# Performance work log

Hardware: AMD Instinct MI355X
Metric: run time of the kernel (lower is better)

The kernel has to match this reference:

```python
import jax, jax.numpy as jnp
import numpy as np

D_MODEL = 1024
N_HEAD = 16
D_K = D_MODEL // N_HEAD
SEQ_LEN = 2048
BATCH = 2
NEG = -1e8


def setup_inputs() -> dict:
    key = jax.random.key(0)
    ks = jax.random.split(key, 8)
    scale = 1.0 / np.sqrt(D_MODEL)
    inp = {
        "input": jax.random.normal(ks[0], (BATCH, SEQ_LEN, D_MODEL), dtype=jnp.float32),
        "mask": jax.random.randint(ks[1], (BATCH, SEQ_LEN), 0, 2) == 1,  # True = masked
        "Wq": jax.random.uniform(ks[2], (D_MODEL, D_MODEL), jnp.float32, -scale, scale),
        "bq": jax.random.uniform(ks[3], (D_MODEL,), jnp.float32, -scale, scale),
        "Wk": jax.random.uniform(ks[4], (D_MODEL, D_MODEL), jnp.float32, -scale, scale),
        "bk": jax.random.uniform(ks[5], (D_MODEL,), jnp.float32, -scale, scale),
        "Wv": jax.random.uniform(ks[6], (D_MODEL, D_MODEL), jnp.float32, -scale, scale),
        "bv": jax.random.uniform(ks[7], (D_MODEL,), jnp.float32, -scale, scale),
    }
    return inp


def reference(input, mask, Wq, bq, Wk, bk, Wv, bv):
    B, S, D = input.shape
    # nn.Linear: y = x @ W^T + b
    def split_heads(x):
        return x.reshape(B, S, N_HEAD, D_K).transpose(0, 2, 1, 3)  # [B,H,S,d_k]

    Q = split_heads(input @ Wq.T + bq)
    K = split_heads(input @ Wk.T + bk)
    V = split_heads(input @ Wv.T + bv)

    scores = jnp.einsum('bhqd,bhkd->bhqk', Q, K) / jnp.sqrt(jnp.float32(D_K))
    # mask [B,S] broadcast over heads and query positions (key mask)
    scores = jnp.where(mask[:, None, None, :], NEG, scores)
    attn = jax.nn.softmax(scores, axis=-1)
    out = jnp.einsum('bhqk,bhkd->bhqd', attn, V)  # [B,H,S,d_k]
    return out.transpose(0, 2, 1, 3).reshape(B, S, D)
```

## Files before the change

### kernel.cpp

```cpp
#include <hip/hip_runtime.h>
#include <hip/hip_bf16.h>
#include <math.h>

#define D_MODEL 1024
#define NH 16
#define DK 64
#define SEQ 2048
#define BATCH 2
#define MTOT (BATCH * SEQ)

typedef unsigned short u16;
typedef unsigned int u32;
typedef short bf16x8 __attribute__((ext_vector_type(8)));
typedef short bf16x4 __attribute__((ext_vector_type(4)));
typedef float f32x4 __attribute__((ext_vector_type(4)));

static constexpr float NEGV2 = -1e8f * 1.44269504089f;
static constexpr float SCL2  = 0.125f * 1.44269504089f;

__device__ __forceinline__ u16 f2bf(float f) {
    union { float f; u32 u; } v; v.f = f;
    u32 r = v.u + 0x7FFFu + ((v.u >> 16) & 1u);
    return (u16)(r >> 16);
}

__device__ __forceinline__ float fexp2(float x) {
#if __has_builtin(__builtin_amdgcn_exp2f)
    return __builtin_amdgcn_exp2f(x);
#else
    return __expf(x * 0.69314718056f);
#endif
}

__device__ __forceinline__ u32 pack2(float lo, float hi) {
    union { __hip_bfloat162 h; u32 u; } cv;
    cv.h = __float22bfloat162_rn(float2{lo, hi});
    return cv.u;
}

__device__ __forceinline__ f32x4 mfma16(bf16x4 a, bf16x4 b, f32x4 c) {
#if __has_builtin(__builtin_amdgcn_mfma_f32_16x16x16_bf16)
    return __builtin_amdgcn_mfma_f32_16x16x16_bf16(a, b, c, 0, 0, 0);
#else
    return __builtin_amdgcn_mfma_f32_16x16x16bf16_1k(a, b, c, 0, 0, 0);
#endif
}

__device__ __forceinline__ void stage16(const u16* g, u16* lds_per_lane) {
#if __has_builtin(__builtin_amdgcn_global_load_lds)
    __builtin_amdgcn_global_load_lds((const __attribute__((address_space(1))) u32*)g,
                                     (__attribute__((address_space(3))) u32*)lds_per_lane,
                                     16, 0, 0);
#else
    *(uint4*)lds_per_lane = *(const uint4*)g;
#endif
}

__global__ __launch_bounds__(256) void convert_bf16(
    const float* __restrict__ X, const float* __restrict__ Wq,
    const float* __restrict__ Wk, const float* __restrict__ Wv,
    u16* __restrict__ Xb, u16* __restrict__ Wb)
{
    const int NX = MTOT * D_MODEL / 4;
    const int NW = D_MODEL * D_MODEL / 4;
    int i = blockIdx.x * 256 + threadIdx.x;
    if (i >= NX + 3 * NW) return;
    float4 v; u16* dst;
    if (i < NX)             { v = ((const float4*)X )[i];            dst = Xb + (size_t)i * 4; }
    else if (i < NX + NW)   { v = ((const float4*)Wq)[i - NX];       dst = Wb + (size_t)(i - NX) * 4; }
    else if (i < NX + 2*NW) { v = ((const float4*)Wk)[i - NX - NW];  dst = Wb + (size_t)NW * 4 + (size_t)(i - NX - NW) * 4; }
    else                    { v = ((const float4*)Wv)[i - NX - 2*NW];dst = Wb + (size_t)NW * 8 + (size_t)(i - NX - 2*NW) * 4; }
    ushort4 o;
    o.x = f2bf(v.x); o.y = f2bf(v.y); o.z = f2bf(v.z); o.w = f2bf(v.w);
    *(ushort4*)dst = o;
}

__global__ __launch_bounds__(256, 2) void proj_mfma(
    const u16* __restrict__ Xb, const u16* __restrict__ Wb,
    const float* __restrict__ bq, const float* __restrict__ bk, const float* __restrict__ bv,
    u16* __restrict__ Qb, u16* __restrict__ Kb, u16* __restrict__ Vb)
{
    __shared__ u16 As[128 * 32];
    __shared__ u16 Bs[128 * 32];

    const int which = blockIdx.z;
    const u16* __restrict__ W = Wb + (size_t)which * D_MODEL * D_MODEL;
    const float* __restrict__ bias = which == 0 ? bq : (which == 1 ? bk : bv);
    u16* __restrict__ Out = which == 0 ? Qb : (which == 1 ? Kb : Vb);

    const int m0 = blockIdx.x * 128, n0 = blockIdx.y * 128;
    const int tid = threadIdx.x, lane = tid & 63, w = tid >> 6;
    const int quad = lane >> 4, l15 = lane & 15;
    const int wr = w >> 1, wc = w & 1;

    f32x4 acc[4][4];
#pragma unroll
    for (int i = 0; i < 4; i++)
#pragma unroll
        for (int j = 0; j < 4; j++) acc[i][j] = (f32x4)0.0f;

    const int srow = 32 * w + (lane >> 2);
    const int scol = (lane & 3) * 8;

    for (int k0 = 0; k0 < D_MODEL; k0 += 32) {
#pragma unroll
        for (int t = 0; t < 2; t++) {
            stage16(Xb + (size_t)(m0 + srow + 16 * t) * D_MODEL + k0 + scol,
                    &As[(32 * w + 16 * t) * 32 + lane * 8]);
            stage16(W + (size_t)(n0 + srow + 16 * t) * D_MODEL + k0 + scol,
                    &Bs[(32 * w + 16 * t) * 32 + lane * 8]);
        }
        __syncthreads();
        bf16x8 af[4], bfr[4];
#pragma unroll
        for (int i = 0; i < 4; i++)
            af[i] = *(const bf16x8*)&As[(wr * 64 + i * 16 + l15) * 32 + quad * 8];
#pragma unroll
        for (int j = 0; j < 4; j++)
            bfr[j] = *(const bf16x8*)&Bs[(wc * 64 + j * 16 + l15) * 32 + quad * 8];
#pragma unroll
        for (int i = 0; i < 4; i++)
#pragma unroll
            for (int j = 0; j < 4; j++)
                acc[i][j] = __builtin_amdgcn_mfma_f32_16x16x32_bf16(af[i], bfr[j], acc[i][j], 0, 0, 0);
        __syncthreads();
    }

    float bj[4];
#pragma unroll
    for (int j = 0; j < 4; j++) bj[j] = bias[n0 + wc * 64 + j * 16 + l15];
#pragma unroll
    for (int i = 0; i < 4; i++) {
#pragma unroll
        for (int j = 0; j < 4; j++) {
#pragma unroll
            for (int r = 0; r < 4; r++) {
                int m = m0 + wr * 64 + i * 16 + quad * 4 + r;
                int n = n0 + wc * 64 + j * 16 + l15;
                int b = m >> 11, s = m & (SEQ - 1);
                int h = n >> 6, d = n & 63;
                Out[(((size_t)b * NH + h) * SEQ + s) * DK + d] = f2bf(acc[i][j][r] + bj[j]);
            }
        }
    }
}

__global__ __launch_bounds__(256, 2) void attn_mfma(
    const u16* __restrict__ Qg, const u16* __restrict__ Kg, const u16* __restrict__ Vg,
    const int* __restrict__ mask, float* __restrict__ out)
{
    constexpr int PADK = 72, PADV = 72;
    __shared__ u16 Ks[2][64 * PADK];
    __shared__ u16 Vt[2][64 * PADV];
    __shared__ float mads[SEQ];

    const int qt0 = blockIdx.x, h = blockIdx.y, b = blockIdx.z;
    const int tid = threadIdx.x, lane = tid & 63, w = tid >> 6;
    const int quad = lane >> 4, l15 = lane & 15;
    const size_t bh = (size_t)b * NH + h;
    const u16* __restrict__ Qp = Qg + (bh * SEQ + qt0 * 128) * DK;
    const u16* __restrict__ Kp = Kg + bh * SEQ * DK;
    const u16* __restrict__ Vp = Vg + bh * SEQ * DK;
    const int* __restrict__ mp = mask + b * SEQ;

    for (int i = tid; i < SEQ; i += 256) mads[i] = mp[i] ? NEGV2 : 0.0f;

    const int q0 = w * 32;
    bf16x8 qf[2][2];
#pragma unroll
    for (int qt = 0; qt < 2; qt++)
#pragma unroll
        for (int half = 0; half < 2; half++)
            qf[qt][half] = *(const bf16x8*)(Qp + (size_t)(q0 + qt * 16 + l15) * DK + half * 32 + quad * 8);

    const int skey = tid & 63, sdk = (tid >> 6) * 16;
    const int vkp2 = (tid & 31) * 2, vd0 = (tid >> 5) * 8;

    {
        const u16* kr = Kp + (size_t)skey * DK + sdk;
        bf16x8 k0 = *(const bf16x8*)kr, k1 = *(const bf16x8*)(kr + 8);
        u16* kd = &Ks[0][skey * PADK + sdk];
        *(bf16x8*)kd = k0; *(bf16x8*)(kd + 8) = k1;
        const u16* vr = Vp + (size_t)vkp2 * DK + vd0;
        bf16x8 v0 = *(const bf16x8*)vr, v1 = *(const bf16x8*)(vr + DK);
#pragma unroll
        for (int i = 0; i < 8; i++)
            *(u32*)&Vt[0][(vd0 + i) * PADV + vkp2] = (u32)(u16)v0[i] | ((u32)(u16)v1[i] << 16);
    }
    __syncthreads();

    f32x4 O[4][2];
    f32x4 sacc[2];
#pragma unroll
    for (int dt = 0; dt < 4; dt++)
#pragma unroll
        for (int qt = 0; qt < 2; qt++) O[dt][qt] = (f32x4)0.0f;
    sacc[0] = (f32x4)0.0f; sacc[1] = (f32x4)0.0f;

    for (int kt = 0; kt < SEQ / 64; kt++) {
        const int bb = kt & 1;
        bf16x8 nk0, nk1, nv0, nv1;
        if (kt < SEQ / 64 - 1) {
            const u16* kr = Kp + (size_t)((kt + 1) * 64 + skey) * DK + sdk;
            nk0 = *(const bf16x8*)kr; nk1 = *(const bf16x8*)(kr + 8);
            const u16* vr = Vp + (size_t)((kt + 1) * 64 + vkp2) * DK + vd0;
            nv0 = *(const bf16x8*)vr; nv1 = *(const bf16x8*)(vr + DK);
        }

        f32x4 St[4][2];
#pragma unroll
        for (int ktl = 0; ktl < 4; ktl++) {
            bf16x8 kf0 = *(const bf16x8*)&Ks[bb][(ktl * 16 + l15) * PADK + quad * 8];
            bf16x8 kf1 = *(const bf16x8*)&Ks[bb][(ktl * 16 + l15) * PADK + 32 + quad * 8];
#pragma unroll
            for (int qt = 0; qt < 2; qt++) {
                f32x4 acc = (f32x4)0.0f;
                acc = __builtin_amdgcn_mfma_f32_16x16x32_bf16(kf0, qf[qt][0], acc, 0, 0, 0);
                acc = __builtin_amdgcn_mfma_f32_16x16x32_bf16(kf1, qf[qt][1], acc, 0, 0, 0);
                St[ktl][qt] = acc;
            }
        }

#pragma unroll
        for (int ktl = 0; ktl < 4; ktl++) {
            f32x4 ma = *(const f32x4*)&mads[kt * 64 + ktl * 16 + quad * 4];
#pragma unroll
            for (int qt = 0; qt < 2; qt++)
#pragma unroll
                for (int r = 0; r < 4; r++) {
                    float p = fexp2(St[ktl][qt][r] * SCL2 + ma[r]);
                    St[ktl][qt][r] = p;
                    sacc[qt][r] += p;
                }
        }

        bf16x4 pf[4][2];
#pragma unroll
        for (int ktl = 0; ktl < 4; ktl++)
#pragma unroll
            for (int qt = 0; qt < 2; qt++) {
                union { u32 u[2]; bf16x4 v; } pu;
                pu.u[0] = pack2(St[ktl][qt][0], St[ktl][qt][1]);
                pu.u[1] = pack2(St[ktl][qt][2], St[ktl][qt][3]);
                pf[ktl][qt] = pu.v;
            }

#pragma unroll
        for (int ktl = 0; ktl < 4; ktl++)
#pragma unroll
            for (int dt = 0; dt < 4; dt++) {
                bf16x4 vf = *(const bf16x4*)&Vt[bb][(dt * 16 + l15) * PADV + ktl * 16 + quad * 4];
#pragma unroll
                for (int qt = 0; qt < 2; qt++)
                    O[dt][qt] = mfma16(vf, pf[ktl][qt], O[dt][qt]);
            }

        if (kt < SEQ / 64 - 1) {
            u16* kd = &Ks[bb ^ 1][skey * PADK + sdk];
            *(bf16x8*)kd = nk0; *(bf16x8*)(kd + 8) = nk1;
#pragma unroll
            for (int i = 0; i < 8; i++)
                *(u32*)&Vt[bb ^ 1][(vd0 + i) * PADV + vkp2] = (u32)(u16)nv0[i] | ((u32)(u16)nv1[i] << 16);
        }
        __syncthreads();
    }

    float inv[2];
#pragma unroll
    for (int qt = 0; qt < 2; qt++) {
        float s = (sacc[qt][0] + sacc[qt][1]) + (sacc[qt][2] + sacc[qt][3]);
        s += __shfl_xor(s, 16);
        s += __shfl_xor(s, 32);
        inv[qt] = 1.0f / s;
    }
#pragma unroll
    for (int qt = 0; qt < 2; qt++) {
        int q = qt0 * 128 + q0 + qt * 16 + l15;
        float* op = out + ((size_t)b * SEQ + q) * D_MODEL + h * DK;
#pragma unroll
        for (int dt = 0; dt < 4; dt++)
#pragma unroll
            for (int r = 0; r < 4; r++)
                op[dt * 16 + quad * 4 + r] = O[dt][qt][r] * inv[qt];
    }
}

extern "C" void kernel_launch(void* const* d_in, const int* in_sizes, int n_in,
                              void* d_out, int out_size, void* d_ws, size_t ws_size,
                              hipStream_t stream)
{
    const float* X  = (const float*)d_in[0];
    const int* mask = (const int*)d_in[1];
    const float* Wq = (const float*)d_in[2];
    const float* bq = (const float*)d_in[3];
    const float* Wk = (const float*)d_in[4];
    const float* bk = (const float*)d_in[5];
    const float* Wv = (const float*)d_in[6];
    const float* bv = (const float*)d_in[7];
    float* out = (float*)d_out;

    u16* Xb = (u16*)d_ws;
    u16* Wb = Xb + (size_t)MTOT * D_MODEL;
    u16* Qb = Wb + (size_t)3 * D_MODEL * D_MODEL;
    u16* Kb = Qb + (size_t)BATCH * NH * SEQ * DK;
    u16* Vb = Kb + (size_t)BATCH * NH * SEQ * DK;

    const int ncvt = (MTOT * D_MODEL + 3 * D_MODEL * D_MODEL) / 4;
    convert_bf16<<<(ncvt + 255) / 256, 256, 0, stream>>>(X, Wq, Wk, Wv, Xb, Wb);
    proj_mfma<<<dim3(MTOT / 128, D_MODEL / 128, 3), 256, 0, stream>>>(Xb, Wb, bq, bk, bv, Qb, Kb, Vb);
    attn_mfma<<<dim3(SEQ / 128, NH, BATCH), 256, 0, stream>>>(Qb, Kb, Vb, mask, out);
}
```

Measured before the change: 174.6 us.

## Shrink attention blocks to 64 queries, precompute mask bias, swizzle projection grid

```diff
diff --git a/kernel.cpp b/kernel.cpp
--- a/kernel.cpp
+++ b/kernel.cpp
@@ -59,12 +59,23 @@
 __global__ __launch_bounds__(256) void convert_bf16(
     const float* __restrict__ X, const float* __restrict__ Wq,
     const float* __restrict__ Wk, const float* __restrict__ Wv,
-    u16* __restrict__ Xb, u16* __restrict__ Wb)
+    const int* __restrict__ mask,
+    u16* __restrict__ Xb, u16* __restrict__ Wb, float* __restrict__ madsg)
 {
     const int NX = MTOT * D_MODEL / 4;
     const int NW = D_MODEL * D_MODEL / 4;
+    const int NM = MTOT / 4;
     int i = blockIdx.x * 256 + threadIdx.x;
-    if (i >= NX + 3 * NW) return;
+    if (i >= NX + 3 * NW + NM) return;
+    if (i >= NX + 3 * NW) {
+        int j = i - NX - 3 * NW;
+        int4 mi = ((const int4*)mask)[j];
+        float4 o;
+        o.x = mi.x ? NEGV2 : 0.0f; o.y = mi.y ? NEGV2 : 0.0f;
+        o.z = mi.z ? NEGV2 : 0.0f; o.w = mi.w ? NEGV2 : 0.0f;
+        ((float4*)madsg)[j] = o;
+        return;
+    }
     float4 v; u16* dst;
     if (i < NX)             { v = ((const float4*)X )[i];            dst = Xb + (size_t)i * 4; }
     else if (i < NX + NW)   { v = ((const float4*)Wq)[i - NX];       dst = Wb + (size_t)(i - NX) * 4; }
@@ -83,12 +94,17 @@
     __shared__ u16 As[128 * 32];
     __shared__ u16 Bs[128 * 32];
 
-    const int which = blockIdx.z;
-    const u16* __restrict__ W = Wb + (size_t)which * D_MODEL * D_MODEL;
-    const float* __restrict__ bias = which == 0 ? bq : (which == 1 ? bk : bv);
-    u16* __restrict__ Out = which == 0 ? Qb : (which == 1 ? Kb : Vb);
-
-    const int m0 = blockIdx.x * 128, n0 = blockIdx.y * 128;
+    const int id = blockIdx.x + 32 * blockIdx.y + 256 * blockIdx.z;
+    const int swz = (id & 7) * 96 + (id >> 3);
+    const int xm = swz & 31;
+    const int yn = (swz >> 5) & 7;
+    const int zi = swz >> 8;
+
+    const u16* __restrict__ W = Wb + (size_t)zi * D_MODEL * D_MODEL;
+    const float* __restrict__ bias = zi == 0 ? bq : (zi == 1 ? bk : bv);
+    u16* __restrict__ Out = zi == 0 ? Qb : (zi == 1 ? Kb : Vb);
+
+    const int m0 = xm * 128, n0 = yn * 128;
     const int tid = threadIdx.x, lane = tid & 63, w = tid >> 6;
     const int quad = lane >> 4, l15 = lane & 15;
     const int wr = w >> 1, wc = w & 1;
@@ -145,25 +161,22 @@
     }
 }
 
-__global__ __launch_bounds__(256, 2) void attn_mfma(
+__global__ __launch_bounds__(128, 2) void attn_mfma(
     const u16* __restrict__ Qg, const u16* __restrict__ Kg, const u16* __restrict__ Vg,
-    const int* __restrict__ mask, float* __restrict__ out)
+    const float* __restrict__ madsg, float* __restrict__ out)
 {
     constexpr int PADK = 72, PADV = 72;
     __shared__ u16 Ks[2][64 * PADK];
     __shared__ u16 Vt[2][64 * PADV];
-    __shared__ float mads[SEQ];
 
     const int qt0 = blockIdx.x, h = blockIdx.y, b = blockIdx.z;
     const int tid = threadIdx.x, lane = tid & 63, w = tid >> 6;
     const int quad = lane >> 4, l15 = lane & 15;
     const size_t bh = (size_t)b * NH + h;
-    const u16* __restrict__ Qp = Qg + (bh * SEQ + qt0 * 128) * DK;
+    const u16* __restrict__ Qp = Qg + (bh * SEQ + qt0 * 64) * DK;
     const u16* __restrict__ Kp = Kg + bh * SEQ * DK;
     const u16* __restrict__ Vp = Vg + bh * SEQ * DK;
-    const int* __restrict__ mp = mask + b * SEQ;
-
-    for (int i = tid; i < SEQ; i += 256) mads[i] = mp[i] ? NEGV2 : 0.0f;
+    const float* __restrict__ mp = madsg + b * SEQ;
 
     const int q0 = w * 32;
     bf16x8 qf[2][2];
@@ -173,19 +186,22 @@
         for (int half = 0; half < 2; half++)
             qf[qt][half] = *(const bf16x8*)(Qp + (size_t)(q0 + qt * 16 + l15) * DK + half * 32 + quad * 8);
 
-    const int skey = tid & 63, sdk = (tid >> 6) * 16;
-    const int vkp2 = (tid & 31) * 2, vd0 = (tid >> 5) * 8;
+    const int skey = tid & 63, sdk = (tid >> 6) * 32;
+    const int vkp2 = (tid & 31) * 2, vd0 = (tid >> 5) * 16;
 
     {
         const u16* kr = Kp + (size_t)skey * DK + sdk;
-        bf16x8 k0 = *(const bf16x8*)kr, k1 = *(const bf16x8*)(kr + 8);
-        u16* kd = &Ks[0][skey * PADK + sdk];
-        *(bf16x8*)kd = k0; *(bf16x8*)(kd + 8) = k1;
+#pragma unroll
+        for (int j = 0; j < 4; j++)
+            *(bf16x8*)&Ks[0][skey * PADK + sdk + 8 * j] = *(const bf16x8*)(kr + 8 * j);
         const u16* vr = Vp + (size_t)vkp2 * DK + vd0;
-        bf16x8 v0 = *(const bf16x8*)vr, v1 = *(const bf16x8*)(vr + DK);
-#pragma unroll
-        for (int i = 0; i < 8; i++)
-            *(u32*)&Vt[0][(vd0 + i) * PADV + vkp2] = (u32)(u16)v0[i] | ((u32)(u16)v1[i] << 16);
+        bf16x8 v0a = *(const bf16x8*)vr,        v0b = *(const bf16x8*)(vr + 8);
+        bf16x8 v1a = *(const bf16x8*)(vr + DK), v1b = *(const bf16x8*)(vr + DK + 8);
+#pragma unroll
+        for (int i = 0; i < 8; i++) {
+            *(u32*)&Vt[0][(vd0 + i) * PADV + vkp2]     = (u32)(u16)v0a[i] | ((u32)(u16)v1a[i] << 16);
+            *(u32*)&Vt[0][(vd0 + 8 + i) * PADV + vkp2] = (u32)(u16)v0b[i] | ((u32)(u16)v1b[i] << 16);
+        }
     }
     __syncthreads();
 
@@ -199,12 +215,14 @@
 
     for (int kt = 0; kt < SEQ / 64; kt++) {
         const int bb = kt & 1;
-        bf16x8 nk0, nk1, nv0, nv1;
+        bf16x8 nk[4], nv0a, nv0b, nv1a, nv1b;
         if (kt < SEQ / 64 - 1) {
             const u16* kr = Kp + (size_t)((kt + 1) * 64 + skey) * DK + sdk;
-            nk0 = *(const bf16x8*)kr; nk1 = *(const bf16x8*)(kr + 8);
+#pragma unroll
+            for (int j = 0; j < 4; j++) nk[j] = *(const bf16x8*)(kr + 8 * j);
             const u16* vr = Vp + (size_t)((kt + 1) * 64 + vkp2) * DK + vd0;
-            nv0 = *(const bf16x8*)vr; nv1 = *(const bf16x8*)(vr + DK);
+            nv0a = *(const bf16x8*)vr;        nv0b = *(const bf16x8*)(vr + 8);
+            nv1a = *(const bf16x8*)(vr + DK); nv1b = *(const bf16x8*)(vr + DK + 8);
         }
 
         f32x4 St[4][2];
@@ -223,7 +241,7 @@
 
 #pragma unroll
         for (int ktl = 0; ktl < 4; ktl++) {
-            f32x4 ma = *(const f32x4*)&mads[kt * 64 + ktl * 16 + quad * 4];
+            f32x4 ma = *(const f32x4*)&mp[kt * 64 + ktl * 16 + quad * 4];
 #pragma unroll
             for (int qt = 0; qt < 2; qt++)
 #pragma unroll
@@ -256,11 +274,14 @@
             }
 
         if (kt < SEQ / 64 - 1) {
-            u16* kd = &Ks[bb ^ 1][skey * PADK + sdk];
-            *(bf16x8*)kd = nk0; *(bf16x8*)(kd + 8) = nk1;
-#pragma unroll
-            for (int i = 0; i < 8; i++)
-                *(u32*)&Vt[bb ^ 1][(vd0 + i) * PADV + vkp2] = (u32)(u16)nv0[i] | ((u32)(u16)nv1[i] << 16);
+#pragma unroll
+            for (int j = 0; j < 4; j++)
+                *(bf16x8*)&Ks[bb ^ 1][skey * PADK + sdk + 8 * j] = nk[j];
+#pragma unroll
+            for (int i = 0; i < 8; i++) {
+                *(u32*)&Vt[bb ^ 1][(vd0 + i) * PADV + vkp2]     = (u32)(u16)nv0a[i] | ((u32)(u16)nv1a[i] << 16);
+                *(u32*)&Vt[bb ^ 1][(vd0 + 8 + i) * PADV + vkp2] = (u32)(u16)nv0b[i] | ((u32)(u16)nv1b[i] << 16);
+            }
         }
         __syncthreads();
     }
@@ -275,7 +296,7 @@
     }
 #pragma unroll
     for (int qt = 0; qt < 2; qt++) {
-        int q = qt0 * 128 + q0 + qt * 16 + l15;
+        int q = qt0 * 64 + q0 + qt * 16 + l15;
         float* op = out + ((size_t)b * SEQ + q) * D_MODEL + h * DK;
 #pragma unroll
         for (int dt = 0; dt < 4; dt++)
@@ -304,9 +325,10 @@
     u16* Qb = Wb + (size_t)3 * D_MODEL * D_MODEL;
     u16* Kb = Qb + (size_t)BATCH * NH * SEQ * DK;
     u16* Vb = Kb + (size_t)BATCH * NH * SEQ * DK;
-
-    const int ncvt = (MTOT * D_MODEL + 3 * D_MODEL * D_MODEL) / 4;
-    convert_bf16<<<(ncvt + 255) / 256, 256, 0, stream>>>(X, Wq, Wk, Wv, Xb, Wb);
+    float* madsg = (float*)(Vb + (size_t)BATCH * NH * SEQ * DK);
+
+    const int ncvt = (MTOT * D_MODEL + 3 * D_MODEL * D_MODEL + MTOT) / 4;
+    convert_bf16<<<(ncvt + 255) / 256, 256, 0, stream>>>(X, Wq, Wk, Wv, mask, Xb, Wb, madsg);
     proj_mfma<<<dim3(MTOT / 128, D_MODEL / 128, 3), 256, 0, stream>>>(Xb, Wb, bq, bk, bv, Qb, Kb, Vb);
-    attn_mfma<<<dim3(SEQ / 128, NH, BATCH), 256, 0, stream>>>(Qb, Kb, Vb, mask, out);
-}
+    attn_mfma<<<dim3(SEQ / 64, NH, BATCH), 128, 0, stream>>>(Qb, Kb, Vb, madsg, out);
+}
```

After: 188.5 us. +8.0%, slower.
